# Kernel tuning notes

Measured on AMD Instinct MI355X. Metric: run time of the kernel, lower is better.

## Reference

```python
import jax, jax.numpy as jnp
import numpy as np

N_G, K = 1024, 64
n_G, k = 32, 8          # n_G = sqrt(N_G), k = sqrt(K)
m = n_G * k             # 256
M = N_G * K             # 65536

def _mask_indices(k):
    # concentric square rings of a k x k grid; ring 0 = outermost
    ii, jj = np.meshgrid(np.arange(k), np.arange(k), indexing='ij')
    d = np.minimum(np.minimum(ii, jj), np.minimum(k - 1 - ii, k - 1 - jj))
    rings = [(d == r) for r in range((k + 1) // 2)]
    groups = np.array_split(np.arange(len(rings)), 3)  # outer / inter / inner ring groups
    merged = [np.any(np.stack([rings[i] for i in g]), axis=0) for g in groups]
    outer, inter, inner = merged
    flat = lambda msk: np.nonzero(msk.ravel())[0]
    return flat(inner), flat(inter), flat(outer)

IDX_INNER, IDX_INTER, IDX_OUTER = _mask_indices(k)  # sizes 4, 12, 48

def setup_inputs() -> dict:
    key = jax.random.key(0)
    ks = jax.random.split(key, 13)
    p = lambda kk, sh: 0.05 * jax.random.normal(kk, sh, dtype=jnp.float32)
    return {
        'pgi': jax.random.normal(ks[0], (32, M, 3), dtype=jnp.float32),
        'W_lift': p(ks[1], (3, 32)),   'b_lift': p(ks[2], (32,)),
        'W_code': p(ks[3], (96, 128)), 'b_code': p(ks[4], (128,)),
        'W_h1': p(ks[5], (128, 64)),   'b_h1': p(ks[6], (64,)),
        'W_h2': p(ks[7], (64, 32)),    'b_h2': p(ks[8], (32,)),
        'W_h3': p(ks[9], (32, 16)),    'b_h3': p(ks[10], (16,)),
        'W_h4': p(ks[11], (16, 3)),    'b_h4': jnp.zeros((3,), jnp.float32),
    }

def _lift_max(pts, W, b):
    # pts: [B, N_G, n_sel, 3] -> SMLP(3->32, leakyrelu 0.2) -> max over points
    h = jax.nn.leaky_relu(jnp.einsum('bgpc,cd->bgpd', pts, W) + b, 0.2)
    return h.max(axis=2)  # [B, N_G, 32]

def reference(pgi, W_lift, b_lift, W_code, b_code, W_h1, b_h1, W_h2, b_h2, W_h3, b_h3, W_h4, b_h4):
    B = pgi.shape[0]
    # pgi [B, M, 3] is a row-major m x m grid; partition into N_G blocks of k x k points
    grid = pgi.reshape(B, n_G, k, n_G, k, 3)
    blocks = grid.transpose(0, 1, 3, 2, 4, 5).reshape(B, N_G, K, 3)
    v_inner = _lift_max(blocks[:, :, IDX_INNER], W_lift, b_lift)
    v_inter = _lift_max(blocks[:, :, IDX_INTER], W_lift, b_lift)
    v_outer = _lift_max(blocks[:, :, IDX_OUTER], W_lift, b_lift)
    v = jnp.concatenate([v_inner, v_inter, v_outer], axis=-1)   # [B, N_G, 96]
    v_code = jax.nn.leaky_relu(v @ W_code + b_code, 0.2)        # [B, N_G, 128]
    h = jax.nn.relu(v_code @ W_h1 + b_h1)
    h = jax.nn.relu(h @ W_h2 + b_h2)
    h = jax.nn.relu(h @ W_h3 + b_h3)
    return h @ W_h4 + b_h4                                      # guidance_pts [B, N_G, 3]
```

## Files before the change

### kernel.cpp

```cpp
#include <hip/hip_runtime.h>
#include <math.h>


typedef _Float16 h8 __attribute__((ext_vector_type(8)));
typedef float    f4 __attribute__((ext_vector_type(4)));

constexpr int WCT_O = 0;
constexpr int W1T_O = 12288;
constexpr int W2T_O = 20480;
constexpr int W3T_O = 22528;
constexpr int WS_N  = 23040;

constexpr int SVH = 104;
constexpr int SCH = 136;
constexpr int S1H = 72;
constexpr int S2H = 40;
constexpr int S3H = 24;
constexpr int H3O = 32 * S2H;

__global__ __launch_bounds__(256)
void cvt_weights(const float* __restrict__ Wc, const float* __restrict__ W1,
                 const float* __restrict__ W2, const float* __restrict__ W3,
                 _Float16* __restrict__ ws16)
{
    const int i = blockIdx.x * 256 + threadIdx.x;
    float v;
    if (i < 12288) {
        const int n = i / 96, k = i - n * 96;
        v = Wc[k * 128 + n];
    } else if (i < 20480) {
        const int j = i - 12288, n = j >> 7, k = j & 127;
        v = W1[k * 64 + n];
    } else if (i < 22528) {
        const int j = i - 20480, n = j >> 6, k = j & 63;
        v = W2[k * 32 + n];
    } else {
        const int j = i - 22528, n = j >> 5, k = j & 31;
        v = W3[k * 16 + n];
    }
    ws16[i] = (_Float16)v;
}

__global__ __launch_bounds__(256, 4)
void flatnet_fused(const float* __restrict__ pgi,
                   const float* __restrict__ Wl, const float* __restrict__ bl,
                   const _Float16* __restrict__ ws16,
                   const float* __restrict__ bc, const float* __restrict__ b1,
                   const float* __restrict__ b2, const float* __restrict__ b3,
                   const float* __restrict__ W4, const float* __restrict__ b4,
                   float* __restrict__ out)
{
    __shared__ __align__(16) _Float16 sV[32 * SVH];
    __shared__ __align__(16) _Float16 sC[32 * SCH];

    const int t    = threadIdx.x;
    const int blk  = blockIdx.x;
    const int lane = t & 63;
    const int wv   = t >> 6;
    const int l15  = lane & 15;
    const int lq   = lane >> 4;

    {
        const int ln = t >> 3;
        const int q  = t & 7;
        const int dq = (q & 3) * 8;
        const int h  = q >> 2;
        const int gn = blk * 32 + ln;
        const int b  = gn >> 10;
        const int g  = gn & 1023;
        const int gi = g >> 5, gj = g & 31;

        float w0[8], w1[8], w2[8], bb[8];
        #pragma unroll
        for (int d = 0; d < 8; ++d) {
            w0[d] = Wl[dq + d];
            w1[d] = Wl[32 + dq + d];
            w2[d] = Wl[64 + dq + d];
            bb[d] = bl[dq + d];
        }

        float gm[3][8];
        #pragma unroll
        for (int gg = 0; gg < 3; ++gg)
            #pragma unroll
            for (int d = 0; d < 8; ++d) gm[gg][d] = -INFINITY;

        constexpr int GT4[4][8] = {
            {2,2,2,2,2,2,2,2},
            {2,2,2,2,2,2,2,2},
            {2,2,1,1,1,1,2,2},
            {2,2,1,0,0,1,2,2},
        };

        const size_t rowbase = (size_t)b * 65536 + ((size_t)gi * 8) * 256 + (size_t)gj * 8;
        #pragma unroll
        for (int pi = 0; pi < 4; ++pi) {
            const int prow = h ? (7 - pi) : pi;
            const float4* src = (const float4*)(pgi + (rowbase + (size_t)prow * 256) * 3);
            float f[24];
            #pragma unroll
            for (int l = 0; l < 6; ++l) {
                const float4 v = src[l];
                f[l*4+0] = v.x; f[l*4+1] = v.y; f[l*4+2] = v.z; f[l*4+3] = v.w;
            }
            #pragma unroll
            for (int pj = 0; pj < 8; ++pj) {
                const int grp = GT4[pi][pj];
                const float x = f[pj*3], y = f[pj*3+1], z = f[pj*3+2];
                #pragma unroll
                for (int d = 0; d < 8; ++d) {
                    float v = fmaf(x, w0[d], bb[d]);
                    v = fmaf(y, w1[d], v);
                    v = fmaf(z, w2[d], v);
                    gm[grp][d] = fmaxf(gm[grp][d], v);
                }
            }
        }
        #pragma unroll
        for (int gg = 0; gg < 3; ++gg)
            #pragma unroll
            for (int d = 0; d < 8; ++d)
                gm[gg][d] = fmaxf(gm[gg][d], __shfl_xor(gm[gg][d], 4));

        if (h == 0) {
            #pragma unroll
            for (int gg = 0; gg < 3; ++gg) {
                h8 hv;
                #pragma unroll
                for (int d = 0; d < 8; ++d) {
                    const float v = gm[gg][d];
                    hv[d] = (_Float16)fmaxf(v, 0.2f * v);
                }
                *(h8*)&sV[ln*SVH + gg*32 + dq] = hv;
            }
        }
    }
    __syncthreads();

    {
        const int nt0 = wv * 2;
        h8 Bf[2][3];
        float bcv[2];
        #pragma unroll
        for (int nn = 0; nn < 2; ++nn) {
            bcv[nn] = bc[(nt0+nn)*16 + l15];
            #pragma unroll
            for (int kq = 0; kq < 3; ++kq)
                Bf[nn][kq] = *(const h8*)&ws16[WCT_O + ((nt0+nn)*16 + l15)*96 + kq*32 + lq*8];
        }
        f4 acc[2][2];
        #pragma unroll
        for (int mt = 0; mt < 2; ++mt)
            #pragma unroll
            for (int nn = 0; nn < 2; ++nn) {
                f4 z = {bcv[nn], bcv[nn], bcv[nn], bcv[nn]};
                acc[mt][nn] = z;
            }
        #pragma unroll
        for (int mt = 0; mt < 2; ++mt) {
            #pragma unroll
            for (int kq = 0; kq < 3; ++kq) {
                const h8 Af = *(const h8*)&sV[(mt*16 + l15)*SVH + kq*32 + lq*8];
                acc[mt][0] = __builtin_amdgcn_mfma_f32_16x16x32_f16(Af, Bf[0][kq], acc[mt][0], 0, 0, 0);
                acc[mt][1] = __builtin_amdgcn_mfma_f32_16x16x32_f16(Af, Bf[1][kq], acc[mt][1], 0, 0, 0);
            }
        }
        __syncthreads();
        #pragma unroll
        for (int mt = 0; mt < 2; ++mt)
            #pragma unroll
            for (int nn = 0; nn < 2; ++nn) {
                const int col = (nt0+nn)*16 + l15;
                #pragma unroll
                for (int r = 0; r < 4; ++r) {
                    const int row = mt*16 + lq*4 + r;
                    const float v = acc[mt][nn][r];
                    sC[row*SCH + col] = (_Float16)fmaxf(v, 0.2f * v);
                }
            }
    }
    __syncthreads();

    {
        h8 Bf[4];
        #pragma unroll
        for (int kq = 0; kq < 4; ++kq)
            Bf[kq] = *(const h8*)&ws16[W1T_O + (wv*16 + l15)*128 + kq*32 + lq*8];
        const float bv = b1[wv*16 + l15];
        f4 acc[2];
        #pragma unroll
        for (int mt = 0; mt < 2; ++mt) { f4 z = {bv,bv,bv,bv}; acc[mt] = z; }
        #pragma unroll
        for (int mt = 0; mt < 2; ++mt)
            #pragma unroll
            for (int kq = 0; kq < 4; ++kq) {
                const h8 Af = *(const h8*)&sC[(mt*16 + l15)*SCH + kq*32 + lq*8];
                acc[mt] = __builtin_amdgcn_mfma_f32_16x16x32_f16(Af, Bf[kq], acc[mt], 0, 0, 0);
            }
        __syncthreads();
        #pragma unroll
        for (int mt = 0; mt < 2; ++mt) {
            const int col = wv*16 + l15;
            #pragma unroll
            for (int r = 0; r < 4; ++r) {
                const int row = mt*16 + lq*4 + r;
                sV[row*S1H + col] = (_Float16)fmaxf(acc[mt][r], 0.f);
            }
        }
    }
    __syncthreads();

    {
        const int mt = wv & 1;
        const int nt = wv >> 1;
        h8 Bf[2];
        #pragma unroll
        for (int kq = 0; kq < 2; ++kq)
            Bf[kq] = *(const h8*)&ws16[W2T_O + (nt*16 + l15)*64 + kq*32 + lq*8];
        const float bv = b2[nt*16 + l15];
        f4 acc = {bv, bv, bv, bv};
        #pragma unroll
        for (int kq = 0; kq < 2; ++kq) {
            const h8 Af = *(const h8*)&sV[(mt*16 + l15)*S1H + kq*32 + lq*8];
            acc = __builtin_amdgcn_mfma_f32_16x16x32_f16(Af, Bf[kq], acc, 0, 0, 0);
        }
        __syncthreads();
        const int col = nt*16 + l15;
        #pragma unroll
        for (int r = 0; r < 4; ++r) {
            const int row = mt*16 + lq*4 + r;
            sC[row*S2H + col] = (_Float16)fmaxf(acc[r], 0.f);
        }
    }
    __syncthreads();

    if (wv < 2) {
        const h8 Bf = *(const h8*)&ws16[W3T_O + l15*32 + lq*8];
        const float bv = b3[l15];
        f4 acc = {bv, bv, bv, bv};
        const h8 Af = *(const h8*)&sC[(wv*16 + l15)*S2H + lq*8];
        acc = __builtin_amdgcn_mfma_f32_16x16x32_f16(Af, Bf, acc, 0, 0, 0);
        #pragma unroll
        for (int r = 0; r < 4; ++r) {
            const int row = wv*16 + lq*4 + r;
            sC[H3O + row*S3H + l15] = (_Float16)fmaxf(acc[r], 0.f);
        }
    }
    __syncthreads();

    if (t < 32) {
        const h8 h0 = *(const h8*)&sC[H3O + t*S3H];
        const h8 h1 = *(const h8*)&sC[H3O + t*S3H + 8];
        float a[16];
        #pragma unroll
        for (int j = 0; j < 8; ++j) { a[j] = (float)h0[j]; a[8+j] = (float)h1[j]; }
        float acc0 = b4[0], acc1 = b4[1], acc2 = b4[2];
        #pragma unroll
        for (int j = 0; j < 16; ++j) {
            acc0 = fmaf(a[j], W4[j*3+0], acc0);
            acc1 = fmaf(a[j], W4[j*3+1], acc1);
            acc2 = fmaf(a[j], W4[j*3+2], acc2);
        }
        const size_t gn = (size_t)blk * 32 + t;
        out[gn*3 + 0] = acc0;
        out[gn*3 + 1] = acc1;
        out[gn*3 + 2] = acc2;
    }
}

extern "C" void kernel_launch(void* const* d_in, const int* in_sizes, int n_in,
                              void* d_out, int out_size, void* d_ws, size_t ws_size,
                              hipStream_t stream)
{
    const float* pgi = (const float*)d_in[0];
    const float* Wl  = (const float*)d_in[1];
    const float* bl  = (const float*)d_in[2];
    const float* Wc  = (const float*)d_in[3];
    const float* bc  = (const float*)d_in[4];
    const float* W1  = (const float*)d_in[5];
    const float* b1  = (const float*)d_in[6];
    const float* W2  = (const float*)d_in[7];
    const float* b2  = (const float*)d_in[8];
    const float* W3  = (const float*)d_in[9];
    const float* b3  = (const float*)d_in[10];
    const float* W4  = (const float*)d_in[11];
    const float* b4  = (const float*)d_in[12];

    _Float16* ws16 = (_Float16*)d_ws;

    hipLaunchKernelGGL(cvt_weights, dim3(90), dim3(256), 0, stream,
                       Wc, W1, W2, W3, ws16);
    hipLaunchKernelGGL(flatnet_fused, dim3(1024), dim3(256), 0, stream,
                       pgi, Wl, bl, ws16, bc, b1, b2, b3, W4, b4,
                       (float*)d_out);
}
```

Baseline: 102.0 us.

## Pre-swizzle weights into MFMA fragment order, hoist loads, drop barriers

```diff
diff --git a/kernel.cpp b/kernel.cpp
--- a/kernel.cpp
+++ b/kernel.cpp
@@ -4,19 +4,13 @@
 
 typedef _Float16 h8 __attribute__((ext_vector_type(8)));
 typedef float    f4 __attribute__((ext_vector_type(4)));
-
-constexpr int WCT_O = 0;
-constexpr int W1T_O = 12288;
-constexpr int W2T_O = 20480;
-constexpr int W3T_O = 22528;
-constexpr int WS_N  = 23040;
 
 constexpr int SVH = 104;
 constexpr int SCH = 136;
 constexpr int S1H = 72;
 constexpr int S2H = 40;
-constexpr int S3H = 24;
-constexpr int H3O = 32 * S2H;
+
+constexpr int P1B = 0, P2B = 24, P3B = 40, P4B = 48;
 
 __global__ __launch_bounds__(256)
 void cvt_weights(const float* __restrict__ Wc, const float* __restrict__ W1,
@@ -24,19 +18,23 @@
                  _Float16* __restrict__ ws16)
 {
     const int i = blockIdx.x * 256 + threadIdx.x;
+    const int fid  = i >> 9;
+    const int r    = i & 511;
+    const int lane = r >> 3, j = r & 7;
+    const int l15  = lane & 15, lq = lane >> 4;
+    const int klo  = lq * 8 + j;
     float v;
-    if (i < 12288) {
-        const int n = i / 96, k = i - n * 96;
-        v = Wc[k * 128 + n];
-    } else if (i < 20480) {
-        const int j = i - 12288, n = j >> 7, k = j & 127;
-        v = W1[k * 64 + n];
-    } else if (i < 22528) {
-        const int j = i - 20480, n = j >> 6, k = j & 63;
-        v = W2[k * 32 + n];
+    if (fid < 24) {
+        const int wv = fid / 6, q = fid % 6, nn = q / 3, kq = q % 3;
+        v = Wc[(kq * 32 + klo) * 128 + (wv * 2 + nn) * 16 + l15];
+    } else if (fid < 40) {
+        const int f2 = fid - 24, wv = f2 >> 2, kq = f2 & 3;
+        v = W1[(kq * 32 + klo) * 64 + wv * 16 + l15];
+    } else if (fid < 48) {
+        const int f3 = fid - 40, wv = f3 >> 1, kq = f3 & 1, nt = wv >> 1;
+        v = W2[(kq * 32 + klo) * 32 + nt * 16 + l15];
     } else {
-        const int j = i - 22528, n = j >> 5, k = j & 31;
-        v = W3[k * 16 + n];
+        v = W3[klo * 16 + l15];
     }
     ws16[i] = (_Float16)v;
 }
@@ -60,6 +58,16 @@
     const int l15  = lane & 15;
     const int lq   = lane >> 4;
 
+    h8 Bf1[2][3];
+    #pragma unroll
+    for (int nn = 0; nn < 2; ++nn)
+        #pragma unroll
+        for (int kq = 0; kq < 3; ++kq)
+            Bf1[nn][kq] = *(const h8*)&ws16[(P1B + wv*6 + nn*3 + kq) * 512 + lane * 8];
+    float bcv[2];
+    bcv[0] = bc[(wv*2 + 0)*16 + l15];
+    bcv[1] = bc[(wv*2 + 1)*16 + l15];
+
     {
         const int ln = t >> 3;
         const int q  = t & 7;
@@ -137,17 +145,13 @@
     }
     __syncthreads();
 
-    {
-        const int nt0 = wv * 2;
-        h8 Bf[2][3];
-        float bcv[2];
-        #pragma unroll
-        for (int nn = 0; nn < 2; ++nn) {
-            bcv[nn] = bc[(nt0+nn)*16 + l15];
-            #pragma unroll
-            for (int kq = 0; kq < 3; ++kq)
-                Bf[nn][kq] = *(const h8*)&ws16[WCT_O + ((nt0+nn)*16 + l15)*96 + kq*32 + lq*8];
-        }
+    h8 Bf2[4];
+    #pragma unroll
+    for (int kq = 0; kq < 4; ++kq)
+        Bf2[kq] = *(const h8*)&ws16[(P2B + wv*4 + kq) * 512 + lane * 8];
+    const float b1v = b1[wv*16 + l15];
+
+    {
         f4 acc[2][2];
         #pragma unroll
         for (int mt = 0; mt < 2; ++mt)
@@ -157,20 +161,18 @@
                 acc[mt][nn] = z;
             }
         #pragma unroll
-        for (int mt = 0; mt < 2; ++mt) {
+        for (int mt = 0; mt < 2; ++mt)
             #pragma unroll
             for (int kq = 0; kq < 3; ++kq) {
                 const h8 Af = *(const h8*)&sV[(mt*16 + l15)*SVH + kq*32 + lq*8];
-                acc[mt][0] = __builtin_amdgcn_mfma_f32_16x16x32_f16(Af, Bf[0][kq], acc[mt][0], 0, 0, 0);
-                acc[mt][1] = __builtin_amdgcn_mfma_f32_16x16x32_f16(Af, Bf[1][kq], acc[mt][1], 0, 0, 0);
-            }
-        }
-        __syncthreads();
+                acc[mt][0] = __builtin_amdgcn_mfma_f32_16x16x32_f16(Af, Bf1[0][kq], acc[mt][0], 0, 0, 0);
+                acc[mt][1] = __builtin_amdgcn_mfma_f32_16x16x32_f16(Af, Bf1[1][kq], acc[mt][1], 0, 0, 0);
+            }
         #pragma unroll
         for (int mt = 0; mt < 2; ++mt)
             #pragma unroll
             for (int nn = 0; nn < 2; ++nn) {
-                const int col = (nt0+nn)*16 + l15;
+                const int col = (wv*2 + nn)*16 + l15;
                 #pragma unroll
                 for (int r = 0; r < 4; ++r) {
                     const int row = mt*16 + lq*4 + r;
@@ -181,23 +183,28 @@
     }
     __syncthreads();
 
-    {
-        h8 Bf[4];
-        #pragma unroll
-        for (int kq = 0; kq < 4; ++kq)
-            Bf[kq] = *(const h8*)&ws16[W1T_O + (wv*16 + l15)*128 + kq*32 + lq*8];
-        const float bv = b1[wv*16 + l15];
+    h8 Bf3[2];
+    #pragma unroll
+    for (int kq = 0; kq < 2; ++kq)
+        Bf3[kq] = *(const h8*)&ws16[(P3B + wv*2 + kq) * 512 + lane * 8];
+    const h8 Bf4 = *(const h8*)&ws16[(P4B + (wv & 1)) * 512 + lane * 8];
+    const float b2v = b2[(wv >> 1)*16 + l15];
+    const float b3v = b3[l15];
+    float w4c[3];
+    #pragma unroll
+    for (int c = 0; c < 3; ++c) w4c[c] = W4[l15*3 + c];
+
+    {
         f4 acc[2];
         #pragma unroll
-        for (int mt = 0; mt < 2; ++mt) { f4 z = {bv,bv,bv,bv}; acc[mt] = z; }
+        for (int mt = 0; mt < 2; ++mt) { f4 z = {b1v,b1v,b1v,b1v}; acc[mt] = z; }
         #pragma unroll
         for (int mt = 0; mt < 2; ++mt)
             #pragma unroll
             for (int kq = 0; kq < 4; ++kq) {
                 const h8 Af = *(const h8*)&sC[(mt*16 + l15)*SCH + kq*32 + lq*8];
-                acc[mt] = __builtin_amdgcn_mfma_f32_16x16x32_f16(Af, Bf[kq], acc[mt], 0, 0, 0);
-            }
-        __syncthreads();
+                acc[mt] = __builtin_amdgcn_mfma_f32_16x16x32_f16(Af, Bf2[kq], acc[mt], 0, 0, 0);
+            }
         #pragma unroll
         for (int mt = 0; mt < 2; ++mt) {
             const int col = wv*16 + l15;
@@ -213,18 +220,12 @@
     {
         const int mt = wv & 1;
         const int nt = wv >> 1;
-        h8 Bf[2];
-        #pragma unroll
-        for (int kq = 0; kq < 2; ++kq)
-            Bf[kq] = *(const h8*)&ws16[W2T_O + (nt*16 + l15)*64 + kq*32 + lq*8];
-        const float bv = b2[nt*16 + l15];
-        f4 acc = {bv, bv, bv, bv};
+        f4 acc = {b2v, b2v, b2v, b2v};
         #pragma unroll
         for (int kq = 0; kq < 2; ++kq) {
             const h8 Af = *(const h8*)&sV[(mt*16 + l15)*S1H + kq*32 + lq*8];
-            acc = __builtin_amdgcn_mfma_f32_16x16x32_f16(Af, Bf[kq], acc, 0, 0, 0);
-        }
-        __syncthreads();
+            acc = __builtin_amdgcn_mfma_f32_16x16x32_f16(Af, Bf3[kq], acc, 0, 0, 0);
+        }
         const int col = nt*16 + l15;
         #pragma unroll
         for (int r = 0; r < 4; ++r) {
@@ -235,36 +236,25 @@
     __syncthreads();
 
     if (wv < 2) {
-        const h8 Bf = *(const h8*)&ws16[W3T_O + l15*32 + lq*8];
-        const float bv = b3[l15];
-        f4 acc = {bv, bv, bv, bv};
+        f4 acc = {b3v, b3v, b3v, b3v};
         const h8 Af = *(const h8*)&sC[(wv*16 + l15)*S2H + lq*8];
-        acc = __builtin_amdgcn_mfma_f32_16x16x32_f16(Af, Bf, acc, 0, 0, 0);
+        acc = __builtin_amdgcn_mfma_f32_16x16x32_f16(Af, Bf4, acc, 0, 0, 0);
         #pragma unroll
         for (int r = 0; r < 4; ++r) {
-            const int row = wv*16 + lq*4 + r;
-            sC[H3O + row*S3H + l15] = (_Float16)fmaxf(acc[r], 0.f);
-        }
-    }
-    __syncthreads();
-
-    if (t < 32) {
-        const h8 h0 = *(const h8*)&sC[H3O + t*S3H];
-        const h8 h1 = *(const h8*)&sC[H3O + t*S3H + 8];
-        float a[16];
-        #pragma unroll
-        for (int j = 0; j < 8; ++j) { a[j] = (float)h0[j]; a[8+j] = (float)h1[j]; }
-        float acc0 = b4[0], acc1 = b4[1], acc2 = b4[2];
-        #pragma unroll
-        for (int j = 0; j < 16; ++j) {
-            acc0 = fmaf(a[j], W4[j*3+0], acc0);
-            acc1 = fmaf(a[j], W4[j*3+1], acc1);
-            acc2 = fmaf(a[j], W4[j*3+2], acc2);
-        }
-        const size_t gn = (size_t)blk * 32 + t;
-        out[gn*3 + 0] = acc0;
-        out[gn*3 + 1] = acc1;
-        out[gn*3 + 2] = acc2;
+            const float h3 = fmaxf(acc[r], 0.f);
+            #pragma unroll
+            for (int c = 0; c < 3; ++c) {
+                float p = h3 * w4c[c];
+                p += __shfl_xor(p, 1);
+                p += __shfl_xor(p, 2);
+                p += __shfl_xor(p, 4);
+                p += __shfl_xor(p, 8);
+                if (l15 == c) {
+                    const int gn = blk*32 + wv*16 + lq*4 + r;
+                    out[gn*3 + c] = p + b4[c];
+                }
+            }
+        }
     }
 }
 
@@ -288,7 +278,7 @@
 
     _Float16* ws16 = (_Float16*)d_ws;
 
-    hipLaunchKernelGGL(cvt_weights, dim3(90), dim3(256), 0, stream,
+    hipLaunchKernelGGL(cvt_weights, dim3(100), dim3(256), 0, stream,
                        Wc, W1, W2, W3, ws16);
     hipLaunchKernelGGL(flatnet_fused, dim3(1024), dim3(256), 0, stream,
                        pgi, Wl, bl, ws16, bc, b1, b2, b3, W4, b4,
```

Result: no change. 101.3 us (-0.7%).
